# Performance work log

Measured on AMD Instinct MI355X. Metric: run time of the kernel, lower is better.

## Reference

```python
import jax, jax.numpy as jnp
import numpy as np

NUM_GROUPS = 32
EPS = 1e-5


def setup_inputs() -> dict:
    key = jax.random.key(0)
    ks = jax.random.split(key, 11)
    B, C, H, W = 4, 512, 64, 64
    s = 1.0 / np.sqrt(C)
    inp = {
        "x": jax.random.normal(ks[0], (B, C, H, W), dtype=jnp.float32),
        "gn_w": jnp.ones((C,), jnp.float32),
        "gn_b": jnp.zeros((C,), jnp.float32),
        "wq": jax.random.uniform(ks[1], (C, C), jnp.float32, -s, s),
        "bq": jax.random.uniform(ks[2], (C,), jnp.float32, -s, s),
        "wk": jax.random.uniform(ks[3], (C, C), jnp.float32, -s, s),
        "bk": jax.random.uniform(ks[4], (C,), jnp.float32, -s, s),
        "wv": jax.random.uniform(ks[5], (C, C), jnp.float32, -s, s),
        "bv": jax.random.uniform(ks[6], (C,), jnp.float32, -s, s),
        "wo": jax.random.uniform(ks[7], (C, C), jnp.float32, -s, s),
        "bo": jax.random.uniform(ks[8], (C,), jnp.float32, -s, s),
    }
    return inp


def reference(x, gn_w, gn_b, wq, bq, wk, bk, wv, bv, wo, bo):
    B, C, H, W = x.shape
    HW = H * W
    # GroupNorm(32, C)
    g = x.reshape(B, NUM_GROUPS, C // NUM_GROUPS, H, W)
    mu = jnp.mean(g, axis=(2, 3, 4), keepdims=True)
    var = jnp.var(g, axis=(2, 3, 4), keepdims=True)
    h = ((g - mu) * jax.lax.rsqrt(var + EPS)).reshape(B, C, H, W)
    h = h * gn_w[None, :, None, None] + gn_b[None, :, None, None]
    # Faithful to original: .view (reshape), NOT permute -> (B, HW, C)
    h = h.reshape(B, HW, C)
    q = h @ wq.T + bq  # (B, HW, C)
    k = h @ wk.T + bk
    v = h @ wv.T + bv
    # Faithful: reshape (not transpose) to (B, C, HW)
    q = q.reshape(B, C, HW)
    k = k.reshape(B, C, HW)
    v = v.reshape(B, C, HW)
    # attn: (B, HW, HW)
    attn = jnp.einsum('bcn,bcm->bnm', q, k)
    attn = jax.nn.softmax(attn, axis=-1)
    # out: (B, C, HW) = v @ attn^T
    out = jnp.einsum('bcm,bnm->bcn', v, attn)
    # transpose to (B, HW, C), out-proj, then reshape back
    out = jnp.swapaxes(out, 1, 2) @ wo.T + bo
    out = out.reshape(B, C, H, W)
    return out + x
```

## Files before the change

kernel.cpp:

```cpp
#include <hip/hip_runtime.h>
#include <hip/hip_fp16.h>
#include <math.h>

constexpr int BATCH = 4;
constexpr int HWDIM = 4096;
constexpr long CNT   = 2097152;
constexpr long ACNT  = 16777216;
constexpr int GSIZE = 65536;
constexpr float GN_EPS = 1e-5f;

typedef __attribute__((ext_vector_type(8))) _Float16 f16x8;
typedef __attribute__((ext_vector_type(4))) float f32x4;

__device__ __forceinline__ unsigned pkf16(float a, float b) {
  __half ha = __float2half(a), hb = __float2half(b);
  return (unsigned)__half_as_ushort(ha) | ((unsigned)__half_as_ushort(hb) << 16);
}
__device__ __forceinline__ float2 up2(unsigned u) {
  __half2 h = *(__half2*)&u;
  return __half22float2(h);
}
__device__ __forceinline__ void gl_lds16(const void* g, void* l) {
  __builtin_amdgcn_global_load_lds((const __attribute__((address_space(1))) unsigned*)g,
                                   (__attribute__((address_space(3))) unsigned*)l, 16, 0, 0);
}
template<int N> __device__ __forceinline__ void wait_vmcnt() {
  if constexpr (N == 0)      asm volatile("s_waitcnt vmcnt(0)" ::: "memory");
  else if constexpr (N == 4) asm volatile("s_waitcnt vmcnt(4)" ::: "memory");
  else if constexpr (N == 6) asm volatile("s_waitcnt vmcnt(6)" ::: "memory");
}

__global__ void gn_stats_kernel(const float* __restrict__ x, float* __restrict__ sacc) {
  const int blk = blockIdx.x;
  const int grp = blk >> 2;
  const float4* p = (const float4*)(x + (long)grp * GSIZE + (long)(blk & 3) * (GSIZE / 4));
  float s = 0.f, q = 0.f;
  for (int i = threadIdx.x; i < GSIZE / 16; i += 256) {
    float4 v = p[i];
    s += (v.x + v.y) + (v.z + v.w);
    q += (v.x * v.x + v.y * v.y) + (v.z * v.z + v.w * v.w);
  }
  #pragma unroll
  for (int o = 32; o > 0; o >>= 1) { s += __shfl_xor(s, o, 64); q += __shfl_xor(q, o, 64); }
  __shared__ float ls[4], lq[4];
  if ((threadIdx.x & 63) == 0) { ls[threadIdx.x >> 6] = s; lq[threadIdx.x >> 6] = q; }
  __syncthreads();
  if (threadIdx.x == 0) {
    atomicAdd(&sacc[grp * 2],     (ls[0] + ls[1]) + (ls[2] + ls[3]));
    atomicAdd(&sacc[grp * 2 + 1], (lq[0] + lq[1]) + (lq[2] + lq[3]));
  }
}

__global__ void gn_norm_f16(const float* __restrict__ x, const float* __restrict__ sacc,
                            const float* __restrict__ gw, const float* __restrict__ gb,
                            unsigned short* __restrict__ h) {
  long i = ((long)blockIdx.x * 256 + threadIdx.x) * 4;
  int c   = (int)((i >> 12) & 511);
  int grp = (int)(i >> 16);
  float S = sacc[grp * 2], Q = sacc[grp * 2 + 1];
  float m = S * (1.f / GSIZE);
  float r = rsqrtf(Q * (1.f / GSIZE) - m * m + GN_EPS);
  float w = gw[c] * r;
  float bia = gb[c] - m * w;
  float4 v = *(const float4*)(x + i);
  *(uint2*)(h + i) = (uint2){ pkf16(v.x * w + bia, v.y * w + bia),
                              pkf16(v.z * w + bia, v.w * w + bia) };
}

__global__ void wcvt(const float* __restrict__ w0, const float* __restrict__ w1,
                     const float* __restrict__ w2, const float* __restrict__ w3,
                     unsigned short* __restrict__ o) {
  const float* src = blockIdx.y == 0 ? w0 : blockIdx.y == 1 ? w1 : blockIdx.y == 2 ? w2 : w3;
  long e = ((long)blockIdx.x * 256 + threadIdx.x) * 4;
  float4 v = *(const float4*)(src + e);
  *(uint2*)(o + (long)blockIdx.y * 262144 + e) = (uint2){ pkf16(v.x, v.y), pkf16(v.z, v.w) };
}

template<int BM, int BN, int NWM, int NWN, int K>
__device__ __forceinline__ void gemm_core(const unsigned short* __restrict__ Ab, long sA,
                                          const unsigned short* __restrict__ Bb, long sB,
                                          unsigned short* LB, const int t, f32x4 (&acc)[8][4]) {
  constexpr int NW   = NWM * NWN;
  constexpr int APW  = BM / 16 / NW;
  constexpr int BPW  = BN / 16 / NW;
  constexpr int L    = APW + BPW;
  constexpr int BUFS = (BM + BN) * 32;
  const int lane = t & 63, w = t >> 6, wm = w & 1, wn = w >> 1;

  auto stage = [&](int buf, int k0) {
    unsigned short* S = LB + buf * BUFS;
    #pragma unroll
    for (int i = 0; i < APW; i++) {
      int fb = w * APW + i;
      gl_lds16(Ab + (long)(fb * 16 + (lane & 15)) * sA + k0 + (lane >> 4) * 8, &S[fb * 512]);
    }
    #pragma unroll
    for (int i = 0; i < BPW; i++) {
      int fb = w * BPW + i;
      gl_lds16(Bb + (long)(fb * 16 + (lane & 15)) * sB + k0 + (lane >> 4) * 8,
               &S[BM * 32 + fb * 512]);
    }
  };
  auto compute = [&](int buf) {
    const unsigned short* As = LB + buf * BUFS;
    const unsigned short* Bs = As + BM * 32;
    f16x8 a[8], b[4];
    #pragma unroll
    for (int i = 0; i < 8; i++) a[i] = *(const f16x8*)&As[((wm * 8 + i) * 64 + lane) * 8];
    #pragma unroll
    for (int j = 0; j < 4; j++) b[j] = *(const f16x8*)&Bs[((wn * 4 + j) * 64 + lane) * 8];
    #pragma unroll
    for (int i = 0; i < 8; i++)
      #pragma unroll
      for (int j = 0; j < 4; j++)
        acc[i][j] = __builtin_amdgcn_mfma_f32_16x16x32_f16(a[i], b[j], acc[i][j], 0, 0, 0);
  };

  stage(0, 0);
  stage(1, 32);
  wait_vmcnt<L>();
  __builtin_amdgcn_s_barrier();
  __builtin_amdgcn_sched_barrier(0);

  #pragma unroll 1
  for (int k0 = 0; k0 + 96 <= K; k0 += 32) {
    const int cur = (k0 >> 5) & 1;
    compute(cur);
    __builtin_amdgcn_sched_barrier(0);
    __builtin_amdgcn_s_barrier();
    stage(cur, k0 + 64);
    wait_vmcnt<L>();
    __builtin_amdgcn_s_barrier();
    __builtin_amdgcn_sched_barrier(0);
  }
  compute(((K - 64) >> 5) & 1);
  wait_vmcnt<0>();
  __builtin_amdgcn_s_barrier();
  __builtin_amdgcn_sched_barrier(0);
  compute(((K - 32) >> 5) & 1);
  __syncthreads();
}

template<int BM, int BN, int NWM, int NWN>
__device__ __forceinline__ void store_f16(unsigned short* LB, f32x4 (&acc)[8][4], const int t,
                                          unsigned short* __restrict__ outp, long sO,
                                          const float* __restrict__ bias) {
  const int lane = t & 63, w = t >> 6, wm = w & 1, wn = w >> 1;
  const int lm = lane & 15, quad = lane >> 4;
  constexpr int TPR = BN / 8;
  constexpr int RPR = (NWM * NWN * 64) / TPR;
  #pragma unroll
  for (int c = 0; c < BM / 64; c++) {
    __syncthreads();
    if (wm == (c >> 1)) {
      #pragma unroll
      for (int i2 = 0; i2 < 4; i2++)
        #pragma unroll
        for (int j = 0; j < 4; j++) {
          int rr = i2 * 16 + quad * 4;
          int cc = wn * 64 + j * 16 + lm;
          float bb = bias ? bias[cc] : 0.f;
          #pragma unroll
          for (int r = 0; r < 4; r++)
            LB[(rr + r) * (BN + 8) + cc] =
                __half_as_ushort(__float2half(acc[(c & 1) * 4 + i2][j][r] + bb));
        }
    }
    __syncthreads();
    #pragma unroll
    for (int k = 0; k < 64 / RPR; k++) {
      int ro = k * RPR + t / TPR;
      int co = (t % TPR) * 8;
      uint4 v = *(const uint4*)&LB[ro * (BN + 8) + co];
      *(uint4*)&outp[(long)(c * 64 + ro) * sO + co] = v;
    }
  }
}

__launch_bounds__(512, 2)
__global__ void proj_qkv(const unsigned short* __restrict__ A, const unsigned short* __restrict__ WF,
                         const float* __restrict__ bq, const float* __restrict__ bk,
                         const float* __restrict__ bv, unsigned short* __restrict__ outq) {
  __shared__ __align__(16) unsigned short LB[32768];
  const int z = blockIdx.z;
  const unsigned short* W = WF + (long)z * 262144;
  const float* bias = z == 0 ? bq : z == 1 ? bk : bv;
  unsigned short* outp = outq + (long)z * 8388608;
  const int m0 = blockIdx.x * 256, n0 = blockIdx.y * 256;
  const int t = threadIdx.x;

  f32x4 acc[8][4];
  #pragma unroll
  for (int i = 0; i < 8; i++)
    #pragma unroll
    for (int j = 0; j < 4; j++) acc[i][j] = (f32x4){0.f, 0.f, 0.f, 0.f};

  gemm_core<256, 256, 2, 4, 512>(A + (long)m0 * 512, 512, W + (long)n0 * 512, 512, LB, t, acc);
  store_f16<256, 256, 2, 4>(LB, acc, t, outp + (long)m0 * 512 + n0, 512, bias + n0);
}

__launch_bounds__(512, 2)
__global__ void proj_out(const unsigned short* __restrict__ A, const unsigned short* __restrict__ W,
                         const float* __restrict__ bias, const float* __restrict__ res,
                         float* __restrict__ outv) {
  __shared__ __align__(16) unsigned short LB[32768];
  const int m0 = blockIdx.x * 256, n0 = blockIdx.y * 256;
  const int t = threadIdx.x;

  f32x4 acc[8][4];
  #pragma unroll
  for (int i = 0; i < 8; i++)
    #pragma unroll
    for (int j = 0; j < 4; j++) acc[i][j] = (f32x4){0.f, 0.f, 0.f, 0.f};

  gemm_core<256, 256, 2, 4, 512>(A + (long)m0 * 512, 512, W + (long)n0 * 512, 512, LB, t, acc);

  const int lane = t & 63, w = t >> 6, wm = w & 1, wn = w >> 1;
  const int lm = lane & 15, quad = lane >> 4;
  #pragma unroll
  for (int i = 0; i < 8; i++)
    #pragma unroll
    for (int j = 0; j < 4; j++) {
      int nn = m0 + wm * 128 + i * 16 + quad * 4;
      int cc = n0 + wn * 64 + j * 16 + lm;
      float bb = bias[cc];
      #pragma unroll
      for (int r = 0; r < 4; r++) {
        long idx = (long)(nn + r) * 512 + cc;
        outv[idx] = acc[i][j][r] + bb + res[idx];
      }
    }
}

__global__ void transpose_f16(const unsigned short* __restrict__ qb,
                              const unsigned short* __restrict__ kb,
                              unsigned short* __restrict__ tr) {
  __shared__ __align__(16) unsigned short ld[64 * 72];
  const int zb = blockIdx.z;
  const int b = zb >> 1;
  const unsigned short* in = (zb & 1 ? kb : qb) + (long)b * CNT;
  unsigned short* o = tr + (long)b * 2 * CNT + (zb & 1 ? CNT : 0);
  const int n0 = blockIdx.x * 64, c0 = blockIdx.y * 64;
  const int t = threadIdx.x;
  unsigned* ld32 = (unsigned*)ld;
  {
    const int p = t >> 3, cg = t & 7;
    uint4 r0 = *(const uint4*)(in + (long)(c0 + 2 * p) * 4096 + n0 + 8 * cg);
    uint4 r1 = *(const uint4*)(in + (long)(c0 + 2 * p + 1) * 4096 + n0 + 8 * cg);
    unsigned aw[4] = { r0.x, r0.y, r0.z, r0.w };
    unsigned bw[4] = { r1.x, r1.y, r1.z, r1.w };
    #pragma unroll
    for (int i = 0; i < 4; i++) {
      ld32[(8 * cg + 2 * i) * 36 + p]     = (aw[i] & 0xFFFFu) | (bw[i] << 16);
      ld32[(8 * cg + 2 * i + 1) * 36 + p] = (aw[i] >> 16) | (bw[i] & 0xFFFF0000u);
    }
  }
  __syncthreads();
  {
    const int n = t >> 2, cg2 = t & 3;
    uint4 o0 = *(const uint4*)(ld + n * 72 + 16 * cg2);
    uint4 o1 = *(const uint4*)(ld + n * 72 + 16 * cg2 + 8);
    *(uint4*)(o + (long)(n0 + n) * 512 + c0 + 16 * cg2)     = o0;
    *(uint4*)(o + (long)(n0 + n) * 512 + c0 + 16 * cg2 + 8) = o1;
  }
}

__launch_bounds__(512, 2)
__global__ void qk_f16(const unsigned short* __restrict__ tr, unsigned short* __restrict__ attn) {
  __shared__ __align__(16) unsigned short LB[32768];
  const int b = blockIdx.z;
  const unsigned short* qT = tr + (long)b * 2 * CNT;
  const unsigned short* kT = qT + CNT;
  const int n0 = blockIdx.x * 256, m0 = blockIdx.y * 256;
  const int t = threadIdx.x;

  f32x4 acc[8][4];
  #pragma unroll
  for (int i = 0; i < 8; i++)
    #pragma unroll
    for (int j = 0; j < 4; j++) acc[i][j] = (f32x4){0.f, 0.f, 0.f, 0.f};

  gemm_core<256, 256, 2, 4, 512>(qT + (long)n0 * 512, 512, kT + (long)m0 * 512, 512, LB, t, acc);
  store_f16<256, 256, 2, 4>(LB, acc, t, attn + (long)b * ACNT + (long)n0 * 4096 + m0, 4096, nullptr);
}

__global__ void softmax_f16ip(unsigned short* __restrict__ attn) {
  unsigned short* p = attn + (long)blockIdx.x * HWDIM;
  const int t = threadIdx.x;
  uint4 u0 = *(const uint4*)(p + t * 16);
  uint4 u1 = *(const uint4*)(p + t * 16 + 8);
  float v[16];
  {
    unsigned uu[8] = { u0.x, u0.y, u0.z, u0.w, u1.x, u1.y, u1.z, u1.w };
    #pragma unroll
    for (int i = 0; i < 8; i++) { float2 f = up2(uu[i]); v[2*i] = f.x; v[2*i+1] = f.y; }
  }
  float mx = -1e30f;
  #pragma unroll
  for (int i = 0; i < 16; i++) mx = fmaxf(mx, v[i]);
  #pragma unroll
  for (int o = 32; o > 0; o >>= 1) mx = fmaxf(mx, __shfl_xor(mx, o, 64));
  __shared__ float rmax[4], rsum[4];
  if ((t & 63) == 0) rmax[t >> 6] = mx;
  __syncthreads();
  mx = fmaxf(fmaxf(rmax[0], rmax[1]), fmaxf(rmax[2], rmax[3]));
  float s = 0.f;
  #pragma unroll
  for (int i = 0; i < 16; i++) { v[i] = __expf(v[i] - mx); s += v[i]; }
  #pragma unroll
  for (int o = 32; o > 0; o >>= 1) s += __shfl_xor(s, o, 64);
  if ((t & 63) == 0) rsum[t >> 6] = s;
  __syncthreads();
  s = (rsum[0] + rsum[1]) + (rsum[2] + rsum[3]);
  float inv = 1.f / s;
  uint4 w0, w1;
  w0.x = pkf16(v[0]*inv,  v[1]*inv);  w0.y = pkf16(v[2]*inv,  v[3]*inv);
  w0.z = pkf16(v[4]*inv,  v[5]*inv);  w0.w = pkf16(v[6]*inv,  v[7]*inv);
  w1.x = pkf16(v[8]*inv,  v[9]*inv);  w1.y = pkf16(v[10]*inv, v[11]*inv);
  w1.z = pkf16(v[12]*inv, v[13]*inv); w1.w = pkf16(v[14]*inv, v[15]*inv);
  *(uint4*)(p + t * 16)     = w0;
  *(uint4*)(p + t * 16 + 8) = w1;
}

__launch_bounds__(256, 2)
__global__ void pv_f16(const unsigned short* __restrict__ P, const unsigned short* __restrict__ V,
                       unsigned short* __restrict__ ot) {
  __shared__ __align__(16) unsigned short LB[24576];
  const int b = blockIdx.z;
  const unsigned short* Pb = P + (long)b * ACNT;
  const unsigned short* Vb = V + (long)b * CNT;
  unsigned short* Ob = ot + (long)b * CNT;
  const int n0 = blockIdx.x * 256, c0 = blockIdx.y * 128;
  const int t = threadIdx.x;

  f32x4 acc[8][4];
  #pragma unroll
  for (int i = 0; i < 8; i++)
    #pragma unroll
    for (int j = 0; j < 4; j++) acc[i][j] = (f32x4){0.f, 0.f, 0.f, 0.f};

  gemm_core<256, 128, 2, 2, 4096>(Pb + (long)n0 * 4096, 4096, Vb + (long)c0 * 4096, 4096, LB, t, acc);
  store_f16<256, 128, 2, 2>(LB, acc, t, Ob + (long)n0 * 512 + c0, 512, nullptr);
}

extern "C" void kernel_launch(void* const* d_in, const int* in_sizes, int n_in,
                              void* d_out, int out_size, void* d_ws, size_t ws_size,
                              hipStream_t stream) {
  (void)in_sizes; (void)n_in; (void)out_size; (void)ws_size;
  const float* x  = (const float*)d_in[0];
  const float* gw = (const float*)d_in[1];
  const float* gb = (const float*)d_in[2];
  const float* wq = (const float*)d_in[3];
  const float* bq = (const float*)d_in[4];
  const float* wk = (const float*)d_in[5];
  const float* bk = (const float*)d_in[6];
  const float* wv = (const float*)d_in[7];
  const float* bv = (const float*)d_in[8];
  const float* wo = (const float*)d_in[9];
  const float* bo = (const float*)d_in[10];
  float* out = (float*)d_out;

  unsigned short* attn = (unsigned short*)d_ws;
  unsigned short* h    = attn;
  unsigned short* qf   = attn + 4 * ACNT;
  unsigned short* kf   = qf + 8388608;
  unsigned short* vf   = kf + 8388608;
  unsigned short* tr   = vf + 8388608;
  unsigned short* ot   = tr + 16777216;
  unsigned short* wf   = ot + 8388608;
  float* sacc = (float*)(wf + 1048576);

  hipMemsetAsync(sacc, 0, 256 * sizeof(float), stream);
  gn_stats_kernel<<<dim3(512), dim3(256), 0, stream>>>(x, sacc);
  gn_norm_f16<<<dim3(8192), dim3(256), 0, stream>>>(x, sacc, gw, gb, h);
  wcvt<<<dim3(256, 4), dim3(256), 0, stream>>>(wq, wk, wv, wo, wf);

  proj_qkv<<<dim3(64, 2, 3), 512, 0, stream>>>(h, wf, bq, bk, bv, qf);

  transpose_f16<<<dim3(64, 8, 8), 256, 0, stream>>>(qf, kf, tr);
  qk_f16<<<dim3(16, 16, 4), 512, 0, stream>>>(tr, attn);
  softmax_f16ip<<<dim3(16384), 256, 0, stream>>>(attn);
  pv_f16<<<dim3(16, 4, 4), 256, 0, stream>>>(attn, vf, ot);

  proj_out<<<dim3(64, 2), 512, 0, stream>>>(ot, wf + 786432, bo, x, out);
}
```

Baseline: 449.7 us.

## Triple-buffer GEMM core with split-phase staging and retile projection/PV kernels

Restructures the shared GEMM main loop to use three LDS buffers. Global-to-LDS loads for A and B are now issued in two halves, interleaved with two half-compute MFMA phases, and s_setprio raises priority during MFMA bursts. The goal is to hide load latency and cut the number of barrier-bound waits per k-step. The projection kernels are retiled to 256x128 with 256 threads, and PV moves to 512 threads with 4x2 waves. This raises LDS use and changes occupancy, and the extra barriers per iteration could add sync cost.

```diff
diff --git a/kernel.cpp b/kernel.cpp
--- a/kernel.cpp
+++ b/kernel.cpp
@@ -26,6 +26,7 @@
 }
 template<int N> __device__ __forceinline__ void wait_vmcnt() {
   if constexpr (N == 0)      asm volatile("s_waitcnt vmcnt(0)" ::: "memory");
+  else if constexpr (N == 3) asm volatile("s_waitcnt vmcnt(3)" ::: "memory");
   else if constexpr (N == 4) asm volatile("s_waitcnt vmcnt(4)" ::: "memory");
   else if constexpr (N == 6) asm volatile("s_waitcnt vmcnt(6)" ::: "memory");
 }
@@ -76,83 +77,108 @@
   *(uint2*)(o + (long)blockIdx.y * 262144 + e) = (uint2){ pkf16(v.x, v.y), pkf16(v.z, v.w) };
 }
 
-template<int BM, int BN, int NWM, int NWN, int K>
+template<int BM, int BN, int NWM, int NWN, int AM, int K>
 __device__ __forceinline__ void gemm_core(const unsigned short* __restrict__ Ab, long sA,
                                           const unsigned short* __restrict__ Bb, long sB,
-                                          unsigned short* LB, const int t, f32x4 (&acc)[8][4]) {
+                                          unsigned short* LB, const int t, f32x4 (&acc)[AM][4]) {
   constexpr int NW   = NWM * NWN;
   constexpr int APW  = BM / 16 / NW;
   constexpr int BPW  = BN / 16 / NW;
   constexpr int L    = APW + BPW;
   constexpr int BUFS = (BM + BN) * 32;
-  const int lane = t & 63, w = t >> 6, wm = w & 1, wn = w >> 1;
-
-  auto stage = [&](int buf, int k0) {
+  const int lane = t & 63, w = t >> 6;
+  const int wm = (NWM == 2) ? (w & 1) : (w >> 1);
+  const int wn = (NWM == 2) ? (w >> 1) : (w & 1);
+
+  auto stageA = [&](int buf, int k0) {
     unsigned short* S = LB + buf * BUFS;
     #pragma unroll
     for (int i = 0; i < APW; i++) {
       int fb = w * APW + i;
       gl_lds16(Ab + (long)(fb * 16 + (lane & 15)) * sA + k0 + (lane >> 4) * 8, &S[fb * 512]);
     }
+  };
+  auto stageB = [&](int buf, int k0) {
+    unsigned short* S = LB + buf * BUFS + BM * 32;
     #pragma unroll
     for (int i = 0; i < BPW; i++) {
       int fb = w * BPW + i;
-      gl_lds16(Bb + (long)(fb * 16 + (lane & 15)) * sB + k0 + (lane >> 4) * 8,
-               &S[BM * 32 + fb * 512]);
+      gl_lds16(Bb + (long)(fb * 16 + (lane & 15)) * sB + k0 + (lane >> 4) * 8, &S[fb * 512]);
     }
   };
-  auto compute = [&](int buf) {
-    const unsigned short* As = LB + buf * BUFS;
+
+  stageA(0, 0); stageB(0, 0);
+  stageA(1, 32); stageB(1, 32);
+  wait_vmcnt<L>();
+  __builtin_amdgcn_s_barrier();
+
+  int cur = 0;
+  #pragma unroll 1
+  for (int k0 = 0; k0 < K; k0 += 32) {
+    const unsigned short* As = LB + cur * BUFS;
     const unsigned short* Bs = As + BM * 32;
-    f16x8 a[8], b[4];
-    #pragma unroll
-    for (int i = 0; i < 8; i++) a[i] = *(const f16x8*)&As[((wm * 8 + i) * 64 + lane) * 8];
-    #pragma unroll
-    for (int j = 0; j < 4; j++) b[j] = *(const f16x8*)&Bs[((wn * 4 + j) * 64 + lane) * 8];
-    #pragma unroll
-    for (int i = 0; i < 8; i++)
+    int nxt = cur + 2; if (nxt >= 3) nxt -= 3;
+    const bool st = (k0 + 64 < K);
+
+    f16x8 a0[AM / 2], b[4];
+    #pragma unroll
+    for (int i = 0; i < AM / 2; i++)
+      a0[i] = *(const f16x8*)&As[((wm * AM + i) * 64 + lane) * 8];
+    #pragma unroll
+    for (int j = 0; j < 4; j++)
+      b[j] = *(const f16x8*)&Bs[((wn * 4 + j) * 64 + lane) * 8];
+    if (st) stageA(nxt, k0 + 64);
+    __builtin_amdgcn_s_barrier();
+    asm volatile("s_waitcnt lgkmcnt(0)" ::: "memory");
+    __builtin_amdgcn_sched_barrier(0);
+    __builtin_amdgcn_s_setprio(1);
+    #pragma unroll
+    for (int i = 0; i < AM / 2; i++)
       #pragma unroll
       for (int j = 0; j < 4; j++)
-        acc[i][j] = __builtin_amdgcn_mfma_f32_16x16x32_f16(a[i], b[j], acc[i][j], 0, 0, 0);
-  };
-
-  stage(0, 0);
-  stage(1, 32);
-  wait_vmcnt<L>();
-  __builtin_amdgcn_s_barrier();
-  __builtin_amdgcn_sched_barrier(0);
-
-  #pragma unroll 1
-  for (int k0 = 0; k0 + 96 <= K; k0 += 32) {
-    const int cur = (k0 >> 5) & 1;
-    compute(cur);
+        acc[i][j] = __builtin_amdgcn_mfma_f32_16x16x32_f16(a0[i], b[j], acc[i][j], 0, 0, 0);
+    __builtin_amdgcn_s_setprio(0);
+    __builtin_amdgcn_s_barrier();
+
+    f16x8 a1[AM / 2];
+    #pragma unroll
+    for (int i = 0; i < AM / 2; i++)
+      a1[i] = *(const f16x8*)&As[((wm * AM + AM / 2 + i) * 64 + lane) * 8];
+    if (st) stageB(nxt, k0 + 64);
+    __builtin_amdgcn_s_barrier();
+    asm volatile("s_waitcnt lgkmcnt(0)" ::: "memory");
     __builtin_amdgcn_sched_barrier(0);
+    __builtin_amdgcn_s_setprio(1);
+    #pragma unroll
+    for (int i = 0; i < AM / 2; i++)
+      #pragma unroll
+      for (int j = 0; j < 4; j++)
+        acc[AM / 2 + i][j] =
+            __builtin_amdgcn_mfma_f32_16x16x32_f16(a1[i], b[j], acc[AM / 2 + i][j], 0, 0, 0);
+    __builtin_amdgcn_s_setprio(0);
+    if (st) wait_vmcnt<L>(); else wait_vmcnt<0>();
     __builtin_amdgcn_s_barrier();
-    stage(cur, k0 + 64);
-    wait_vmcnt<L>();
-    __builtin_amdgcn_s_barrier();
-    __builtin_amdgcn_sched_barrier(0);
-  }
-  compute(((K - 64) >> 5) & 1);
-  wait_vmcnt<0>();
-  __builtin_amdgcn_s_barrier();
-  __builtin_amdgcn_sched_barrier(0);
-  compute(((K - 32) >> 5) & 1);
+    cur = cur + 1; if (cur >= 3) cur = 0;
+  }
   __syncthreads();
 }
 
-template<int BM, int BN, int NWM, int NWN>
-__device__ __forceinline__ void store_f16(unsigned short* LB, f32x4 (&acc)[8][4], const int t,
+template<int BM, int BN, int NWM, int NWN, int AM>
+__device__ __forceinline__ void store_f16(unsigned short* LB, f32x4 (&acc)[AM][4], const int t,
                                           unsigned short* __restrict__ outp, long sO,
                                           const float* __restrict__ bias) {
-  const int lane = t & 63, w = t >> 6, wm = w & 1, wn = w >> 1;
+  const int lane = t & 63, w = t >> 6;
+  const int wm = (NWM == 2) ? (w & 1) : (w >> 1);
+  const int wn = (NWM == 2) ? (w >> 1) : (w & 1);
   const int lm = lane & 15, quad = lane >> 4;
+  constexpr int NT  = NWM * NWN * 64;
   constexpr int TPR = BN / 8;
-  constexpr int RPR = (NWM * NWN * 64) / TPR;
+  constexpr int RPR = NT / TPR;
+  constexpr int CPW = AM / 4;
   #pragma unroll
   for (int c = 0; c < BM / 64; c++) {
     __syncthreads();
-    if (wm == (c >> 1)) {
+    if (wm == c / CPW) {
       #pragma unroll
       for (int i2 = 0; i2 < 4; i2++)
         #pragma unroll
@@ -163,7 +189,7 @@
           #pragma unroll
           for (int r = 0; r < 4; r++)
             LB[(rr + r) * (BN + 8) + cc] =
-                __half_as_ushort(__float2half(acc[(c & 1) * 4 + i2][j][r] + bb));
+                __half_as_ushort(__float2half(acc[(c % CPW) * 4 + i2][j][r] + bb));
         }
     }
     __syncthreads();
@@ -177,16 +203,16 @@
   }
 }
 
-__launch_bounds__(512, 2)
+__launch_bounds__(256, 2)
 __global__ void proj_qkv(const unsigned short* __restrict__ A, const unsigned short* __restrict__ WF,
                          const float* __restrict__ bq, const float* __restrict__ bk,
                          const float* __restrict__ bv, unsigned short* __restrict__ outq) {
-  __shared__ __align__(16) unsigned short LB[32768];
+  __shared__ __align__(16) unsigned short LB[36864];
   const int z = blockIdx.z;
   const unsigned short* W = WF + (long)z * 262144;
   const float* bias = z == 0 ? bq : z == 1 ? bk : bv;
   unsigned short* outp = outq + (long)z * 8388608;
-  const int m0 = blockIdx.x * 256, n0 = blockIdx.y * 256;
+  const int m0 = blockIdx.x * 256, n0 = blockIdx.y * 128;
   const int t = threadIdx.x;
 
   f32x4 acc[8][4];
@@ -195,16 +221,16 @@
     #pragma unroll
     for (int j = 0; j < 4; j++) acc[i][j] = (f32x4){0.f, 0.f, 0.f, 0.f};
 
-  gemm_core<256, 256, 2, 4, 512>(A + (long)m0 * 512, 512, W + (long)n0 * 512, 512, LB, t, acc);
-  store_f16<256, 256, 2, 4>(LB, acc, t, outp + (long)m0 * 512 + n0, 512, bias + n0);
-}
-
-__launch_bounds__(512, 2)
+  gemm_core<256, 128, 2, 2, 8, 512>(A + (long)m0 * 512, 512, W + (long)n0 * 512, 512, LB, t, acc);
+  store_f16<256, 128, 2, 2, 8>(LB, acc, t, outp + (long)m0 * 512 + n0, 512, bias + n0);
+}
+
+__launch_bounds__(256, 2)
 __global__ void proj_out(const unsigned short* __restrict__ A, const unsigned short* __restrict__ W,
                          const float* __restrict__ bias, const float* __restrict__ res,
                          float* __restrict__ outv) {
-  __shared__ __align__(16) unsigned short LB[32768];
-  const int m0 = blockIdx.x * 256, n0 = blockIdx.y * 256;
+  __shared__ __align__(16) unsigned short LB[36864];
+  const int m0 = blockIdx.x * 256, n0 = blockIdx.y * 128;
   const int t = threadIdx.x;
 
   f32x4 acc[8][4];
@@ -213,7 +239,7 @@
     #pragma unroll
     for (int j = 0; j < 4; j++) acc[i][j] = (f32x4){0.f, 0.f, 0.f, 0.f};
 
-  gemm_core<256, 256, 2, 4, 512>(A + (long)m0 * 512, 512, W + (long)n0 * 512, 512, LB, t, acc);
+  gemm_core<256, 128, 2, 2, 8, 512>(A + (long)m0 * 512, 512, W + (long)n0 * 512, 512, LB, t, acc);
 
   const int lane = t & 63, w = t >> 6, wm = w & 1, wn = w >> 1;
   const int lm = lane & 15, quad = lane >> 4;
@@ -267,7 +293,7 @@
 
 __launch_bounds__(512, 2)
 __global__ void qk_f16(const unsigned short* __restrict__ tr, unsigned short* __restrict__ attn) {
-  __shared__ __align__(16) unsigned short LB[32768];
+  __shared__ __align__(16) unsigned short LB[49152];
   const int b = blockIdx.z;
   const unsigned short* qT = tr + (long)b * 2 * CNT;
   const unsigned short* kT = qT + CNT;
@@ -280,8 +306,9 @@
     #pragma unroll
     for (int j = 0; j < 4; j++) acc[i][j] = (f32x4){0.f, 0.f, 0.f, 0.f};
 
-  gemm_core<256, 256, 2, 4, 512>(qT + (long)n0 * 512, 512, kT + (long)m0 * 512, 512, LB, t, acc);
-  store_f16<256, 256, 2, 4>(LB, acc, t, attn + (long)b * ACNT + (long)n0 * 4096 + m0, 4096, nullptr);
+  gemm_core<256, 256, 2, 4, 8, 512>(qT + (long)n0 * 512, 512, kT + (long)m0 * 512, 512, LB, t, acc);
+  store_f16<256, 256, 2, 4, 8>(LB, acc, t, attn + (long)b * ACNT + (long)n0 * 4096 + m0, 4096,
+                               nullptr);
 }
 
 __global__ void softmax_f16ip(unsigned short* __restrict__ attn) {
@@ -322,10 +349,10 @@
   *(uint4*)(p + t * 16 + 8) = w1;
 }
 
-__launch_bounds__(256, 2)
+__launch_bounds__(512, 2)
 __global__ void pv_f16(const unsigned short* __restrict__ P, const unsigned short* __restrict__ V,
                        unsigned short* __restrict__ ot) {
-  __shared__ __align__(16) unsigned short LB[24576];
+  __shared__ __align__(16) unsigned short LB[36864];
   const int b = blockIdx.z;
   const unsigned short* Pb = P + (long)b * ACNT;
   const unsigned short* Vb = V + (long)b * CNT;
@@ -333,14 +360,15 @@
   const int n0 = blockIdx.x * 256, c0 = blockIdx.y * 128;
   const int t = threadIdx.x;
 
-  f32x4 acc[8][4];
-  #pragma unroll
-  for (int i = 0; i < 8; i++)
+  f32x4 acc[4][4];
+  #pragma unroll
+  for (int i = 0; i < 4; i++)
     #pragma unroll
     for (int j = 0; j < 4; j++) acc[i][j] = (f32x4){0.f, 0.f, 0.f, 0.f};
 
-  gemm_core<256, 128, 2, 2, 4096>(Pb + (long)n0 * 4096, 4096, Vb + (long)c0 * 4096, 4096, LB, t, acc);
-  store_f16<256, 128, 2, 2>(LB, acc, t, Ob + (long)n0 * 512 + c0, 512, nullptr);
+  gemm_core<256, 128, 4, 2, 4, 4096>(Pb + (long)n0 * 4096, 4096, Vb + (long)c0 * 4096, 4096,
+                                     LB, t, acc);
+  store_f16<256, 128, 4, 2, 4>(LB, acc, t, Ob + (long)n0 * 512 + c0, 512, nullptr);
 }
 
 extern "C" void kernel_launch(void* const* d_in, const int* in_sizes, int n_in,
@@ -375,12 +403,12 @@
   gn_norm_f16<<<dim3(8192), dim3(256), 0, stream>>>(x, sacc, gw, gb, h);
   wcvt<<<dim3(256, 4), dim3(256), 0, stream>>>(wq, wk, wv, wo, wf);
 
-  proj_qkv<<<dim3(64, 2, 3), 512, 0, stream>>>(h, wf, bq, bk, bv, qf);
+  proj_qkv<<<dim3(64, 4, 3), 256, 0, stream>>>(h, wf, bq, bk, bv, qf);
 
   transpose_f16<<<dim3(64, 8, 8), 256, 0, stream>>>(qf, kf, tr);
   qk_f16<<<dim3(16, 16, 4), 512, 0, stream>>>(tr, attn);
   softmax_f16ip<<<dim3(16384), 256, 0, stream>>>(attn);
-  pv_f16<<<dim3(16, 4, 4), 256, 0, stream>>>(attn, vf, ot);
-
-  proj_out<<<dim3(64, 2), 512, 0, stream>>>(ot, wf + 786432, bo, x, out);
-}
+  pv_f16<<<dim3(16, 4, 4), 512, 0, stream>>>(attn, vf, ot);
+
+  proj_out<<<dim3(64, 4), 256, 0, stream>>>(ot, wf + 786432, bo, x, out);
+}
```

Measured after the change: 434.1 us. 1.04x faster.
